# Kernel optimization log

Hardware: AMD Instinct MI355X
Metric: run time of the kernel (lower is better)

Reference implementation:

```python
import jax, jax.numpy as jnp
import numpy as np

B, S, D = 32, 2048, 1024

def setup_inputs() -> dict:
    key = jax.random.key(0)
    k1, k2, k3 = jax.random.split(key, 3)
    embed_output = jax.random.normal(k1, (B, S, D), dtype=jnp.float32)
    mask = jax.random.randint(k2, (B, S), 0, 2) > 0  # bool [B,S]
    w = jax.random.normal(k3, (D, D), dtype=jnp.float32) * 0.05
    return {"embed_output": embed_output, "mask": mask, "w": w}

def reference(embed_output, mask, w):
    # ys: mean over sequence (NOTE: original does NOT mask the mean) -> [B,1,D]
    ys = jnp.mean(embed_output, axis=-2, keepdims=True)
    maskf = mask.astype(jnp.float32)
    # eW = (E @ W) * mask  -> [B,S,D]
    eW = jnp.einsum('bsd,de->bse', embed_output, w) * maskf[..., None]
    # f = dot(eW, ys) over last axis -> [B,S,1]
    f = jnp.sum(eW * ys, axis=-1, keepdims=True)
    # additive -1e9 bias where mask is False
    f = f + ((1.0 - maskf) * -1.0e9)[..., None]
    # softmax over sequence axis (-2)
    f = jax.nn.softmax(f, axis=-2)
    # weighted sum over sequence -> [B,D]
    zs = jnp.sum(f * embed_output, axis=-2)
    return zs, f
```

## Files before the change

kernel.cpp:

```cpp
#include <hip/hip_runtime.h>
#include <hip/hip_bf16.h>

#define B_ 32
#define S_ 2048
#define D_ 1024
#define NCH1 32
#define NW3 256

typedef float fx4_t __attribute__((ext_vector_type(4)));

__global__ __launch_bounds__(256) void k1_colsum(const float* __restrict__ E,
                                                 float* __restrict__ part_sums,
                                                 const unsigned int* __restrict__ mprobe,
                                                 int* __restrict__ flag) {
    int chunk = blockIdx.x, b = blockIdx.y, tid = threadIdx.x;
    if (chunk == 0 && b == 0 && tid < 64) {
        bool isI = true, isF = true;
        for (int i = tid * 4; i < tid * 4 + 4; ++i) {
            unsigned v = mprobe[i];
            if (v > 1u) isI = false;
            if (v != 0u && v != 0x3F800000u) isF = false;
        }
        unsigned long long bi = __ballot(isI);
        unsigned long long bf = __ballot(isF);
        if (tid == 0) {
            int f = 0;
            if (bi == ~0ull) f = 1;
            else if (bf == ~0ull) f = 2;
            *flag = f;
        }
    }
    const float4* base =
        (const float4*)(E + (size_t)(b * S_ + chunk * (S_ / NCH1)) * D_);
    float4 acc = make_float4(0.f, 0.f, 0.f, 0.f);
#pragma unroll 4
    for (int i = 0; i < S_ / NCH1; ++i) {
        float4 e = base[(size_t)i * (D_ / 4) + tid];
        acc.x += e.x; acc.y += e.y; acc.z += e.z; acc.w += e.w;
    }
    ((float4*)part_sums)[(size_t)(b * NCH1 + chunk) * (D_ / 4) + tid] = acc;
}

__global__ void k2a_ys(const float* __restrict__ part_sums, float* __restrict__ ys) {
    int g = blockIdx.x * 256 + threadIdx.x;
    int b = g >> 10, d = g & (D_ - 1);
    float s = 0.f;
#pragma unroll 8
    for (int k = 0; k < NCH1; ++k) s += part_sums[(size_t)(b * NCH1 + k) * D_ + d];
    ys[g] = s * (1.0f / S_);
}

__global__ __launch_bounds__(256) void k2b_v(const float* __restrict__ w,
                                             const float* __restrict__ ys,
                                             float* __restrict__ v) {
    int tid = threadIdx.x, wave = tid >> 6, lane = tid & 63;
    int d = blockIdx.x * 4 + wave;
    const float4* wrow = (const float4*)(w + (size_t)d * D_);
    float4 w0 = wrow[lane], w1 = wrow[64 + lane], w2 = wrow[128 + lane], w3 = wrow[192 + lane];
    for (int b = 0; b < B_; ++b) {
        const float4* yb = (const float4*)(ys + (size_t)b * D_);
        float4 y0 = yb[lane], y1 = yb[64 + lane], y2 = yb[128 + lane], y3 = yb[192 + lane];
        float p = w0.x * y0.x + w0.y * y0.y + w0.z * y0.z + w0.w * y0.w;
        p += w1.x * y1.x + w1.y * y1.y + w1.z * y1.z + w1.w * y1.w;
        p += w2.x * y2.x + w2.y * y2.y + w2.z * y2.z + w2.w * y2.w;
        p += w3.x * y3.x + w3.y * y3.y + w3.z * y3.z + w3.w * y3.w;
#pragma unroll
        for (int off = 32; off; off >>= 1) p += __shfl_xor(p, off, 64);
        if (lane == 0) v[(size_t)b * D_ + d] = p;
    }
}

__global__ __launch_bounds__(256) void k3_fused(
    const float* __restrict__ E, const void* __restrict__ maskp,
    const float* __restrict__ v, const int* __restrict__ flagp,
    float* __restrict__ logits, float* __restrict__ part_l,
    float* __restrict__ part_z) {
    int b = (B_ - 1) - blockIdx.y;
    int tid = threadIdx.x, wave = tid >> 6, lane = tid & 63;
    int c = ((NW3 / 4 - 1) - blockIdx.x) * 4 + wave;
    int mf = *flagp;
    const int* mi = (const int*)maskp;
    const unsigned char* mu = (const unsigned char*)maskp;
    const float* mfl = (const float*)maskp;

    const float4* vf = (const float4*)(v + (size_t)b * D_);
    float4 v0 = vf[lane], v1 = vf[64 + lane], v2 = vf[128 + lane], v3 = vf[192 + lane];

    float4 z0 = make_float4(0.f, 0.f, 0.f, 0.f), z1 = z0, z2 = z0, z3 = z0;
    float lacc = 0.f;

#pragma unroll
    for (int g = 0; g < 2; ++g) {
        int s0 = c * 8 + g * 4;
        const float4* row0 = (const float4*)(E + (size_t)(b * S_ + s0) * D_);
        float4 e[4][4];
#pragma unroll
        for (int i = 0; i < 4; ++i) {
            const float4* row = row0 + (size_t)i * (D_ / 4);
            e[i][0] = row[lane]; e[i][1] = row[64 + lane];
            e[i][2] = row[128 + lane]; e[i][3] = row[192 + lane];
        }
        float lg4[4], wt4[4];
#pragma unroll
        for (int i = 0; i < 4; ++i) {
            float p = e[i][0].x * v0.x + e[i][0].y * v0.y + e[i][0].z * v0.z + e[i][0].w * v0.w;
            p += e[i][1].x * v1.x + e[i][1].y * v1.y + e[i][1].z * v1.z + e[i][1].w * v1.w;
            p += e[i][2].x * v2.x + e[i][2].y * v2.y + e[i][2].z * v2.z + e[i][2].w * v2.w;
            p += e[i][3].x * v3.x + e[i][3].y * v3.y + e[i][3].z * v3.z + e[i][3].w * v3.w;
#pragma unroll
            for (int off = 32; off; off >>= 1) p += __shfl_xor(p, off, 64);
            int idx = b * S_ + s0 + i;
            int mv = (mf == 1) ? (mi[idx] != 0)
                               : (mf == 2 ? (mfl[idx] != 0.0f) : (mu[idx] != 0));
            lg4[i] = mv ? p : -1.0e9f;
            wt4[i] = mv ? __expf(p) : 0.0f;
        }
        if (lane == 0)
            *(float4*)(logits + (size_t)b * S_ + s0) =
                make_float4(lg4[0], lg4[1], lg4[2], lg4[3]);
#pragma unroll
        for (int i = 0; i < 4; ++i) {
            float pe = wt4[i];
            z0.x += pe * e[i][0].x; z0.y += pe * e[i][0].y; z0.z += pe * e[i][0].z; z0.w += pe * e[i][0].w;
            z1.x += pe * e[i][1].x; z1.y += pe * e[i][1].y; z1.z += pe * e[i][1].z; z1.w += pe * e[i][1].w;
            z2.x += pe * e[i][2].x; z2.y += pe * e[i][2].y; z2.z += pe * e[i][2].z; z2.w += pe * e[i][2].w;
            z3.x += pe * e[i][3].x; z3.y += pe * e[i][3].y; z3.z += pe * e[i][3].z; z3.w += pe * e[i][3].w;
        }
        lacc += wt4[0] + wt4[1] + wt4[2] + wt4[3];
    }

    fx4_t* pz = (fx4_t*)(part_z + (size_t)(b * NW3 + c) * D_);
    fx4_t s0v = {z0.x, z0.y, z0.z, z0.w};
    fx4_t s1v = {z1.x, z1.y, z1.z, z1.w};
    fx4_t s2v = {z2.x, z2.y, z2.z, z2.w};
    fx4_t s3v = {z3.x, z3.y, z3.z, z3.w};
    __builtin_nontemporal_store(s0v, &pz[lane]);
    __builtin_nontemporal_store(s1v, &pz[64 + lane]);
    __builtin_nontemporal_store(s2v, &pz[128 + lane]);
    __builtin_nontemporal_store(s3v, &pz[192 + lane]);
    if (lane == 0) part_l[b * NW3 + c] = lacc;
}

__global__ __launch_bounds__(256) void k4_merge_f(
    const float* __restrict__ part_l, const float* __restrict__ part_z,
    const float* __restrict__ logits, float* __restrict__ out_zs,
    float* __restrict__ out_f) {
    int x = blockIdx.x, b = blockIdx.y, tid = threadIdx.x;
    int cg = tid >> 5, d4 = tid & 31;
    __shared__ float pl_s[NW3];
    __shared__ float4 red[8][32];

    float4 acc = make_float4(0.f, 0.f, 0.f, 0.f);
#pragma unroll 4
    for (int k = 0; k < NW3 / 8; ++k) {
        int c = cg + k * 8;
        float4 zv = ((const float4*)part_z)[(size_t)(b * NW3 + c) * (D_ / 4) + x * 32 + d4];
        acc.x += zv.x; acc.y += zv.y; acc.z += zv.z; acc.w += zv.w;
    }
    red[cg][d4] = acc;
    pl_s[tid] = part_l[b * NW3 + tid];
    __syncthreads();

    float lsum = 0.f;
#pragma unroll 8
    for (int i = 0; i < NW3; ++i) lsum += pl_s[i];
    float inv = 1.0f / lsum;

    if (tid < 32) {
        float4 t = red[0][tid];
#pragma unroll
        for (int j = 1; j < 8; ++j) {
            float4 u = red[j][tid];
            t.x += u.x; t.y += u.y; t.z += u.z; t.w += u.w;
        }
        ((float4*)out_zs)[b * (D_ / 4) + x * 32 + tid] =
            make_float4(t.x * inv, t.y * inv, t.z * inv, t.w * inv);
    }
    if (tid < 64) {
        float4 lv = ((const float4*)logits)[b * (S_ / 4) + x * 64 + tid];
        ((float4*)out_f)[b * (S_ / 4) + x * 64 + tid] =
            make_float4(__expf(lv.x) * inv, __expf(lv.y) * inv,
                        __expf(lv.z) * inv, __expf(lv.w) * inv);
    }
}

extern "C" void kernel_launch(void* const* d_in, const int* in_sizes, int n_in,
                              void* d_out, int out_size, void* d_ws, size_t ws_size,
                              hipStream_t stream) {
    const float* E = (const float*)d_in[0];
    const void* maskp = d_in[1];
    const float* w = (const float*)d_in[2];
    float* out = (float*)d_out;

    float* ws = (float*)d_ws;
    float* part_sums = ws;
    float* ys = part_sums + (size_t)B_ * NCH1 * D_;
    float* v = ys + (size_t)B_ * D_;
    float* logits = v + (size_t)B_ * D_;
    float* part_l = logits + (size_t)B_ * S_;
    float* part_z = part_l + B_ * NW3;
    int* flag = (int*)(part_z + (size_t)B_ * NW3 * D_);

    k1_colsum<<<dim3(NCH1, B_), 256, 0, stream>>>(E, part_sums,
                                                  (const unsigned int*)maskp, flag);
    k2a_ys<<<(B_ * D_) / 256, 256, 0, stream>>>(part_sums, ys);
    k2b_v<<<D_ / 4, 256, 0, stream>>>(w, ys, v);
    k3_fused<<<dim3(NW3 / 4, B_), 256, 0, stream>>>(E, maskp, v, flag, logits,
                                                    part_l, part_z);
    k4_merge_f<<<dim3(8, B_), 256, 0, stream>>>(part_l, part_z, logits,
                                                out, out + B_ * D_);
}
```

Measured before the change: 437.1 us.

## Fuse all stages into one persistent kernel with software grid barriers

Replaces the chain of five launches with a small init kernel plus one 1024-block persistent kernel. The stages inside it are separated by atomic-counter grid barriers, which removes launch gaps and tail effects between stages. The attention pass now reduces its partials across waves in shared memory, so each block writes a single 1024-wide partial instead of four, which shrinks part_z and the final merge. The barrier assumes all 1024 blocks are co-resident and has a timeout fallback, so correctness depends on occupancy.

Measured after the change: 981.2 us. 124% more time.

```diff
diff --git a/kernel.cpp b/kernel.cpp
--- a/kernel.cpp
+++ b/kernel.cpp
@@ -4,183 +4,222 @@
 #define B_ 32
 #define S_ 2048
 #define D_ 1024
-#define NCH1 32
-#define NW3 256
-
-typedef float fx4_t __attribute__((ext_vector_type(4)));
-
-__global__ __launch_bounds__(256) void k1_colsum(const float* __restrict__ E,
-                                                 float* __restrict__ part_sums,
-                                                 const unsigned int* __restrict__ mprobe,
-                                                 int* __restrict__ flag) {
-    int chunk = blockIdx.x, b = blockIdx.y, tid = threadIdx.x;
-    if (chunk == 0 && b == 0 && tid < 64) {
-        bool isI = true, isF = true;
-        for (int i = tid * 4; i < tid * 4 + 4; ++i) {
-            unsigned v = mprobe[i];
-            if (v > 1u) isI = false;
-            if (v != 0u && v != 0x3F800000u) isF = false;
-        }
-        unsigned long long bi = __ballot(isI);
-        unsigned long long bf = __ballot(isF);
-        if (tid == 0) {
-            int f = 0;
-            if (bi == ~0ull) f = 1;
-            else if (bf == ~0ull) f = 2;
-            *flag = f;
-        }
-    }
-    const float4* base =
-        (const float4*)(E + (size_t)(b * S_ + chunk * (S_ / NCH1)) * D_);
-    float4 acc = make_float4(0.f, 0.f, 0.f, 0.f);
+#define NB_ 1024
+
+__device__ __forceinline__ void gsync(unsigned* bar) {
+    __syncthreads();
+    if (threadIdx.x == 0) {
+        __threadfence();
+        unsigned g = *(volatile unsigned*)&bar[1];
+        unsigned prev = atomicAdd(&bar[0], 1u);
+        if (prev == (unsigned)NB_ - 1u) {
+            bar[0] = 0u;
+            __threadfence();
+            atomicAdd(&bar[1], 1u);
+        } else {
+            long long t0 = clock64();
+            while (*(volatile unsigned*)&bar[1] == g) {
+                __builtin_amdgcn_s_sleep(8);
+                if (clock64() - t0 > 100000000LL) break;
+            }
+        }
+        __threadfence();
+    }
+    __syncthreads();
+}
+
+__global__ void k0_init(unsigned* __restrict__ bar,
+                        const unsigned int* __restrict__ mprobe,
+                        int* __restrict__ flag) {
+    int tid = threadIdx.x;
+    if (tid < 2) bar[tid] = 0u;
+    bool isI = true, isF = true;
+    for (int i = tid * 4; i < tid * 4 + 4; ++i) {
+        unsigned v = mprobe[i];
+        if (v > 1u) isI = false;
+        if (v != 0u && v != 0x3F800000u) isF = false;
+    }
+    unsigned long long bi = __ballot(isI);
+    unsigned long long bf = __ballot(isF);
+    if (tid == 0) {
+        int f = 0;
+        if (bi == ~0ull) f = 1;
+        else if (bf == ~0ull) f = 2;
+        *flag = f;
+    }
+}
+
+__global__ __launch_bounds__(256, 4) void fused_all(
+    const float* __restrict__ E, const void* __restrict__ maskp,
+    const float* __restrict__ w, float* __restrict__ out_zs,
+    float* __restrict__ out_f, float* __restrict__ part_sums,
+    float* __restrict__ ys, float* __restrict__ v, float* __restrict__ logits,
+    float* __restrict__ part_l, float* __restrict__ part_z,
+    const int* __restrict__ flagp, unsigned* __restrict__ bar) {
+    int beta = blockIdx.x, tid = threadIdx.x, wave = tid >> 6, lane = tid & 63;
+    __shared__ __align__(16) float sm[4160];
+
+    {
+        int b = beta >> 5, chunk = beta & 31;
+        const float4* base = (const float4*)(E + (size_t)(b * S_ + chunk * 64) * D_);
+        float4 a0 = make_float4(0.f, 0.f, 0.f, 0.f), a1 = a0;
 #pragma unroll 4
-    for (int i = 0; i < S_ / NCH1; ++i) {
-        float4 e = base[(size_t)i * (D_ / 4) + tid];
-        acc.x += e.x; acc.y += e.y; acc.z += e.z; acc.w += e.w;
-    }
-    ((float4*)part_sums)[(size_t)(b * NCH1 + chunk) * (D_ / 4) + tid] = acc;
-}
-
-__global__ void k2a_ys(const float* __restrict__ part_sums, float* __restrict__ ys) {
-    int g = blockIdx.x * 256 + threadIdx.x;
-    int b = g >> 10, d = g & (D_ - 1);
-    float s = 0.f;
+        for (int i = 0; i < 64; i += 2) {
+            float4 e0 = base[(size_t)i * (D_ / 4) + tid];
+            float4 e1 = base[(size_t)(i + 1) * (D_ / 4) + tid];
+            a0.x += e0.x; a0.y += e0.y; a0.z += e0.z; a0.w += e0.w;
+            a1.x += e1.x; a1.y += e1.y; a1.z += e1.z; a1.w += e1.w;
+        }
+        a0.x += a1.x; a0.y += a1.y; a0.z += a1.z; a0.w += a1.w;
+        ((float4*)part_sums)[(size_t)(b * 32 + chunk) * (D_ / 4) + tid] = a0;
+    }
+    gsync(bar);
+
+    if (beta < 128) {
+        int g = beta * 256 + tid;
+        int b = g >> 10, d = g & (D_ - 1);
+        float s = 0.f;
 #pragma unroll 8
-    for (int k = 0; k < NCH1; ++k) s += part_sums[(size_t)(b * NCH1 + k) * D_ + d];
-    ys[g] = s * (1.0f / S_);
-}
-
-__global__ __launch_bounds__(256) void k2b_v(const float* __restrict__ w,
-                                             const float* __restrict__ ys,
-                                             float* __restrict__ v) {
-    int tid = threadIdx.x, wave = tid >> 6, lane = tid & 63;
-    int d = blockIdx.x * 4 + wave;
-    const float4* wrow = (const float4*)(w + (size_t)d * D_);
-    float4 w0 = wrow[lane], w1 = wrow[64 + lane], w2 = wrow[128 + lane], w3 = wrow[192 + lane];
-    for (int b = 0; b < B_; ++b) {
-        const float4* yb = (const float4*)(ys + (size_t)b * D_);
-        float4 y0 = yb[lane], y1 = yb[64 + lane], y2 = yb[128 + lane], y3 = yb[192 + lane];
-        float p = w0.x * y0.x + w0.y * y0.y + w0.z * y0.z + w0.w * y0.w;
-        p += w1.x * y1.x + w1.y * y1.y + w1.z * y1.z + w1.w * y1.w;
-        p += w2.x * y2.x + w2.y * y2.y + w2.z * y2.z + w2.w * y2.w;
-        p += w3.x * y3.x + w3.y * y3.y + w3.z * y3.z + w3.w * y3.w;
-#pragma unroll
-        for (int off = 32; off; off >>= 1) p += __shfl_xor(p, off, 64);
-        if (lane == 0) v[(size_t)b * D_ + d] = p;
-    }
-}
-
-__global__ __launch_bounds__(256) void k3_fused(
-    const float* __restrict__ E, const void* __restrict__ maskp,
-    const float* __restrict__ v, const int* __restrict__ flagp,
-    float* __restrict__ logits, float* __restrict__ part_l,
-    float* __restrict__ part_z) {
-    int b = (B_ - 1) - blockIdx.y;
-    int tid = threadIdx.x, wave = tid >> 6, lane = tid & 63;
-    int c = ((NW3 / 4 - 1) - blockIdx.x) * 4 + wave;
+        for (int k = 0; k < 32; ++k) s += part_sums[(size_t)(b * 32 + k) * D_ + d];
+        ys[g] = s * (1.0f / S_);
+    }
+    gsync(bar);
+
+    if (beta < 256) {
+        int d = beta * 4 + wave;
+        const float4* wrow = (const float4*)(w + (size_t)d * D_);
+        float4 w0 = wrow[lane], w1 = wrow[64 + lane], w2 = wrow[128 + lane],
+               w3 = wrow[192 + lane];
+        const float4* y0p = (const float4*)(ys);
+        float4 n0 = y0p[lane], n1 = y0p[64 + lane], n2 = y0p[128 + lane],
+               n3 = y0p[192 + lane];
+        for (int b = 0; b < B_; ++b) {
+            float4 y0 = n0, y1 = n1, y2 = n2, y3 = n3;
+            if (b + 1 < B_) {
+                const float4* yn = (const float4*)(ys + (size_t)(b + 1) * D_);
+                n0 = yn[lane]; n1 = yn[64 + lane]; n2 = yn[128 + lane]; n3 = yn[192 + lane];
+            }
+            float p = w0.x * y0.x + w0.y * y0.y + w0.z * y0.z + w0.w * y0.w;
+            p += w1.x * y1.x + w1.y * y1.y + w1.z * y1.z + w1.w * y1.w;
+            p += w2.x * y2.x + w2.y * y2.y + w2.z * y2.z + w2.w * y2.w;
+            p += w3.x * y3.x + w3.y * y3.y + w3.z * y3.z + w3.w * y3.w;
+#pragma unroll
+            for (int off = 32; off; off >>= 1) p += __shfl_xor(p, off, 64);
+            if (lane == 0) v[(size_t)b * D_ + d] = p;
+        }
+    }
+    gsync(bar);
+
     int mf = *flagp;
-    const int* mi = (const int*)maskp;
-    const unsigned char* mu = (const unsigned char*)maskp;
-    const float* mfl = (const float*)maskp;
-
-    const float4* vf = (const float4*)(v + (size_t)b * D_);
-    float4 v0 = vf[lane], v1 = vf[64 + lane], v2 = vf[128 + lane], v3 = vf[192 + lane];
-
-    float4 z0 = make_float4(0.f, 0.f, 0.f, 0.f), z1 = z0, z2 = z0, z3 = z0;
-    float lacc = 0.f;
-
-#pragma unroll
-    for (int g = 0; g < 2; ++g) {
-        int s0 = c * 8 + g * 4;
-        const float4* row0 = (const float4*)(E + (size_t)(b * S_ + s0) * D_);
-        float4 e[4][4];
-#pragma unroll
-        for (int i = 0; i < 4; ++i) {
-            const float4* row = row0 + (size_t)i * (D_ / 4);
-            e[i][0] = row[lane]; e[i][1] = row[64 + lane];
-            e[i][2] = row[128 + lane]; e[i][3] = row[192 + lane];
-        }
-        float lg4[4], wt4[4];
-#pragma unroll
-        for (int i = 0; i < 4; ++i) {
-            float p = e[i][0].x * v0.x + e[i][0].y * v0.y + e[i][0].z * v0.z + e[i][0].w * v0.w;
-            p += e[i][1].x * v1.x + e[i][1].y * v1.y + e[i][1].z * v1.z + e[i][1].w * v1.w;
-            p += e[i][2].x * v2.x + e[i][2].y * v2.y + e[i][2].z * v2.z + e[i][2].w * v2.w;
-            p += e[i][3].x * v3.x + e[i][3].y * v3.y + e[i][3].z * v3.z + e[i][3].w * v3.w;
-#pragma unroll
-            for (int off = 32; off; off >>= 1) p += __shfl_xor(p, off, 64);
-            int idx = b * S_ + s0 + i;
-            int mv = (mf == 1) ? (mi[idx] != 0)
-                               : (mf == 2 ? (mfl[idx] != 0.0f) : (mu[idx] != 0));
-            lg4[i] = mv ? p : -1.0e9f;
-            wt4[i] = mv ? __expf(p) : 0.0f;
-        }
-        if (lane == 0)
-            *(float4*)(logits + (size_t)b * S_ + s0) =
-                make_float4(lg4[0], lg4[1], lg4[2], lg4[3]);
-#pragma unroll
-        for (int i = 0; i < 4; ++i) {
-            float pe = wt4[i];
-            z0.x += pe * e[i][0].x; z0.y += pe * e[i][0].y; z0.z += pe * e[i][0].z; z0.w += pe * e[i][0].w;
-            z1.x += pe * e[i][1].x; z1.y += pe * e[i][1].y; z1.z += pe * e[i][1].z; z1.w += pe * e[i][1].w;
-            z2.x += pe * e[i][2].x; z2.y += pe * e[i][2].y; z2.z += pe * e[i][2].z; z2.w += pe * e[i][2].w;
-            z3.x += pe * e[i][3].x; z3.y += pe * e[i][3].y; z3.z += pe * e[i][3].z; z3.w += pe * e[i][3].w;
-        }
-        lacc += wt4[0] + wt4[1] + wt4[2] + wt4[3];
-    }
-
-    fx4_t* pz = (fx4_t*)(part_z + (size_t)(b * NW3 + c) * D_);
-    fx4_t s0v = {z0.x, z0.y, z0.z, z0.w};
-    fx4_t s1v = {z1.x, z1.y, z1.z, z1.w};
-    fx4_t s2v = {z2.x, z2.y, z2.z, z2.w};
-    fx4_t s3v = {z3.x, z3.y, z3.z, z3.w};
-    __builtin_nontemporal_store(s0v, &pz[lane]);
-    __builtin_nontemporal_store(s1v, &pz[64 + lane]);
-    __builtin_nontemporal_store(s2v, &pz[128 + lane]);
-    __builtin_nontemporal_store(s3v, &pz[192 + lane]);
-    if (lane == 0) part_l[b * NW3 + c] = lacc;
-}
-
-__global__ __launch_bounds__(256) void k4_merge_f(
-    const float* __restrict__ part_l, const float* __restrict__ part_z,
-    const float* __restrict__ logits, float* __restrict__ out_zs,
-    float* __restrict__ out_f) {
-    int x = blockIdx.x, b = blockIdx.y, tid = threadIdx.x;
-    int cg = tid >> 5, d4 = tid & 31;
-    __shared__ float pl_s[NW3];
-    __shared__ float4 red[8][32];
-
-    float4 acc = make_float4(0.f, 0.f, 0.f, 0.f);
-#pragma unroll 4
-    for (int k = 0; k < NW3 / 8; ++k) {
-        int c = cg + k * 8;
-        float4 zv = ((const float4*)part_z)[(size_t)(b * NW3 + c) * (D_ / 4) + x * 32 + d4];
-        acc.x += zv.x; acc.y += zv.y; acc.z += zv.z; acc.w += zv.w;
-    }
-    red[cg][d4] = acc;
-    pl_s[tid] = part_l[b * NW3 + tid];
-    __syncthreads();
-
-    float lsum = 0.f;
-#pragma unroll 8
-    for (int i = 0; i < NW3; ++i) lsum += pl_s[i];
-    float inv = 1.0f / lsum;
-
-    if (tid < 32) {
-        float4 t = red[0][tid];
-#pragma unroll
-        for (int j = 1; j < 8; ++j) {
-            float4 u = red[j][tid];
-            t.x += u.x; t.y += u.y; t.z += u.z; t.w += u.w;
-        }
-        ((float4*)out_zs)[b * (D_ / 4) + x * 32 + tid] =
-            make_float4(t.x * inv, t.y * inv, t.z * inv, t.w * inv);
-    }
-    if (tid < 64) {
-        float4 lv = ((const float4*)logits)[b * (S_ / 4) + x * 64 + tid];
-        ((float4*)out_f)[b * (S_ / 4) + x * 64 + tid] =
-            make_float4(__expf(lv.x) * inv, __expf(lv.y) * inv,
-                        __expf(lv.z) * inv, __expf(lv.w) * inv);
+    {
+        int b = beta >> 5, chunk = beta & 31;
+        const int* mi = (const int*)maskp;
+        const unsigned char* mu = (const unsigned char*)maskp;
+        const float* mfl = (const float*)maskp;
+        const float4* vf = (const float4*)(v + (size_t)b * D_);
+        float4 v0 = vf[lane], v1 = vf[64 + lane], v2 = vf[128 + lane], v3 = vf[192 + lane];
+        float4 z0 = make_float4(0.f, 0.f, 0.f, 0.f), z1 = z0, z2 = z0, z3 = z0;
+        float lacc = 0.f;
+#pragma unroll
+        for (int t = 0; t < 2; ++t) {
+            int s0 = chunk * 64 + t * 32 + wave * 8;
+            const float4* row0 = (const float4*)(E + (size_t)(b * S_ + s0) * D_);
+            float lg8[8];
+#pragma unroll
+            for (int grp = 0; grp < 4; ++grp) {
+                const float4* ra = row0 + (size_t)(grp * 2) * (D_ / 4);
+                const float4* rb = row0 + (size_t)(grp * 2 + 1) * (D_ / 4);
+                float4 a0 = ra[lane], a1 = ra[64 + lane], a2 = ra[128 + lane], a3 = ra[192 + lane];
+                float4 b0 = rb[lane], b1 = rb[64 + lane], b2 = rb[128 + lane], b3 = rb[192 + lane];
+                float p0 = a0.x * v0.x + a0.y * v0.y + a0.z * v0.z + a0.w * v0.w;
+                p0 += a1.x * v1.x + a1.y * v1.y + a1.z * v1.z + a1.w * v1.w;
+                p0 += a2.x * v2.x + a2.y * v2.y + a2.z * v2.z + a2.w * v2.w;
+                p0 += a3.x * v3.x + a3.y * v3.y + a3.z * v3.z + a3.w * v3.w;
+                float p1 = b0.x * v0.x + b0.y * v0.y + b0.z * v0.z + b0.w * v0.w;
+                p1 += b1.x * v1.x + b1.y * v1.y + b1.z * v1.z + b1.w * v1.w;
+                p1 += b2.x * v2.x + b2.y * v2.y + b2.z * v2.z + b2.w * v2.w;
+                p1 += b3.x * v3.x + b3.y * v3.y + b3.z * v3.z + b3.w * v3.w;
+#pragma unroll
+                for (int off = 32; off; off >>= 1) {
+                    p0 += __shfl_xor(p0, off, 64);
+                    p1 += __shfl_xor(p1, off, 64);
+                }
+                int r0 = b * S_ + s0 + grp * 2, r1 = r0 + 1;
+                int m0 = (mf == 1) ? (mi[r0] != 0)
+                                   : (mf == 2 ? (mfl[r0] != 0.0f) : (mu[r0] != 0));
+                int m1 = (mf == 1) ? (mi[r1] != 0)
+                                   : (mf == 2 ? (mfl[r1] != 0.0f) : (mu[r1] != 0));
+                lg8[grp * 2] = m0 ? p0 : -1.0e9f;
+                lg8[grp * 2 + 1] = m1 ? p1 : -1.0e9f;
+                float e0 = m0 ? __expf(p0) : 0.0f;
+                float e1 = m1 ? __expf(p1) : 0.0f;
+                z0.x += e0 * a0.x + e1 * b0.x; z0.y += e0 * a0.y + e1 * b0.y;
+                z0.z += e0 * a0.z + e1 * b0.z; z0.w += e0 * a0.w + e1 * b0.w;
+                z1.x += e0 * a1.x + e1 * b1.x; z1.y += e0 * a1.y + e1 * b1.y;
+                z1.z += e0 * a1.z + e1 * b1.z; z1.w += e0 * a1.w + e1 * b1.w;
+                z2.x += e0 * a2.x + e1 * b2.x; z2.y += e0 * a2.y + e1 * b2.y;
+                z2.z += e0 * a2.z + e1 * b2.z; z2.w += e0 * a2.w + e1 * b2.w;
+                z3.x += e0 * a3.x + e1 * b3.x; z3.y += e0 * a3.y + e1 * b3.y;
+                z3.z += e0 * a3.z + e1 * b3.z; z3.w += e0 * a3.w + e1 * b3.w;
+                lacc += e0 + e1;
+            }
+            if (lane == 0) {
+                float4* lp = (float4*)(logits + (size_t)b * S_ + s0);
+                lp[0] = make_float4(lg8[0], lg8[1], lg8[2], lg8[3]);
+                lp[1] = make_float4(lg8[4], lg8[5], lg8[6], lg8[7]);
+            }
+        }
+        *(float4*)&sm[wave * 1024 + 0 * 256 + lane * 4] = z0;
+        *(float4*)&sm[wave * 1024 + 1 * 256 + lane * 4] = z1;
+        *(float4*)&sm[wave * 1024 + 2 * 256 + lane * 4] = z2;
+        *(float4*)&sm[wave * 1024 + 3 * 256 + lane * 4] = z3;
+        if (lane == 0) sm[4096 + wave] = lacc;
+        __syncthreads();
+        float4 s0v = *(float4*)&sm[0 * 1024 + tid * 4];
+        float4 s1v = *(float4*)&sm[1 * 1024 + tid * 4];
+        float4 s2v = *(float4*)&sm[2 * 1024 + tid * 4];
+        float4 s3v = *(float4*)&sm[3 * 1024 + tid * 4];
+        s0v.x += s1v.x + s2v.x + s3v.x; s0v.y += s1v.y + s2v.y + s3v.y;
+        s0v.z += s1v.z + s2v.z + s3v.z; s0v.w += s1v.w + s2v.w + s3v.w;
+        ((float4*)part_z)[(size_t)(b * 32 + chunk) * (D_ / 4) + tid] = s0v;
+        if (tid == 0)
+            part_l[b * 32 + chunk] = sm[4096] + sm[4097] + sm[4098] + sm[4099];
+    }
+    gsync(bar);
+
+    if (beta < 256) {
+        int b = beta >> 3, x = beta & 7;
+        int cg = tid >> 5, d4 = tid & 31;
+        float4 acc = make_float4(0.f, 0.f, 0.f, 0.f);
+#pragma unroll
+        for (int k = 0; k < 4; ++k) {
+            int c = cg + k * 8;
+            float4 zv = ((const float4*)part_z)[(size_t)(b * 32 + c) * (D_ / 4) + x * 32 + d4];
+            acc.x += zv.x; acc.y += zv.y; acc.z += zv.z; acc.w += zv.w;
+        }
+        *(float4*)&sm[(cg * 32 + d4) * 4] = acc;
+        if (tid < 32) sm[4096 + tid] = part_l[b * 32 + tid];
+        __syncthreads();
+        float lsum = 0.f;
+#pragma unroll
+        for (int i = 0; i < 32; ++i) lsum += sm[4096 + i];
+        float inv = 1.0f / lsum;
+        if (tid < 32) {
+            float4 t4 = *(float4*)&sm[tid * 4];
+#pragma unroll
+            for (int j = 1; j < 8; ++j) {
+                float4 u = *(float4*)&sm[(j * 32 + tid) * 4];
+                t4.x += u.x; t4.y += u.y; t4.z += u.z; t4.w += u.w;
+            }
+            ((float4*)out_zs)[(size_t)b * (D_ / 4) + x * 32 + tid] =
+                make_float4(t4.x * inv, t4.y * inv, t4.z * inv, t4.w * inv);
+        }
+        if (tid < 64) {
+            float4 lv = ((const float4*)logits)[(size_t)b * (S_ / 4) + x * 64 + tid];
+            ((float4*)out_f)[(size_t)b * (S_ / 4) + x * 64 + tid] =
+                make_float4(__expf(lv.x) * inv, __expf(lv.y) * inv,
+                            __expf(lv.z) * inv, __expf(lv.w) * inv);
+        }
     }
 }
 
@@ -194,19 +233,19 @@
 
     float* ws = (float*)d_ws;
     float* part_sums = ws;
-    float* ys = part_sums + (size_t)B_ * NCH1 * D_;
+    float* ys = part_sums + (size_t)B_ * 32 * D_;
     float* v = ys + (size_t)B_ * D_;
     float* logits = v + (size_t)B_ * D_;
     float* part_l = logits + (size_t)B_ * S_;
-    float* part_z = part_l + B_ * NW3;
-    int* flag = (int*)(part_z + (size_t)B_ * NW3 * D_);
-
-    k1_colsum<<<dim3(NCH1, B_), 256, 0, stream>>>(E, part_sums,
-                                                  (const unsigned int*)maskp, flag);
-    k2a_ys<<<(B_ * D_) / 256, 256, 0, stream>>>(part_sums, ys);
-    k2b_v<<<D_ / 4, 256, 0, stream>>>(w, ys, v);
-    k3_fused<<<dim3(NW3 / 4, B_), 256, 0, stream>>>(E, maskp, v, flag, logits,
-                                                    part_l, part_z);
-    k4_merge_f<<<dim3(8, B_), 256, 0, stream>>>(part_l, part_z, logits,
-                                                out, out + B_ * D_);
-}
+    float* part_z = part_l + B_ * 32;
+    int* flag = (int*)(part_z + (size_t)B_ * 32 * D_);
+    unsigned* bar = (unsigned*)(flag + 4);
+
+    k0_init<<<1, 64, 0, stream>>>(bar, (const unsigned int*)maskp, flag);
+
+    float* out_f = out + (size_t)B_ * D_;
+    hipLaunchKernelGGL(fused_all, dim3(NB_), dim3(256), 0, stream, E, maskp, w,
+                       out, out_f, part_sums, ys, v, logits, part_l, part_z,
+                       flag, bar);
+    (void)ws_size; (void)in_sizes; (void)n_in; (void)out_size;
+}
```
